# Kernel optimization log

Measured on AMD Instinct MI355X. Metric: run time of the kernel, lower is better.

The kernel has to match this reference:

```python
import jax, jax.numpy as jnp
import numpy as np
import math

B, T_TOK, D, H, L, V, NC, BS = 8, 511, 768, 12, 8, 512, 10, 512

PARAM_NAMES = ['tok_emb','cond_emb','type_emb','pos_emb','ln1_g','ln1_b','Wq','bq','Wk','bk','Wv','bv','Wp','bp','ln2_g','ln2_b','W1','b1','W2','b2','lnf_g','lnf_b','head_w']


def setup_inputs() -> dict:
    key = jax.random.key(0)
    ks = iter(jax.random.split(key, 40))
    def w(shape):
        return jax.random.normal(next(ks), shape, jnp.float32) * 0.02
    inp = {
        'idx': jax.random.randint(next(ks), (B, T_TOK), 0, V),
        'condition': jax.random.randint(next(ks), (B,), 0, NC + 1),
        'tok_emb': w((V, D)),
        'cond_emb': w((NC + 1, D)),
        'type_emb': w((2, D)),
        'pos_emb': w((1, BS, D)),
        'ln1_g': jnp.ones((L, D)), 'ln1_b': jnp.zeros((L, D)),
        'Wq': w((L, D, D)), 'bq': jnp.zeros((L, D)),
        'Wk': w((L, D, D)), 'bk': jnp.zeros((L, D)),
        'Wv': w((L, D, D)), 'bv': jnp.zeros((L, D)),
        'Wp': w((L, D, D)), 'bp': jnp.zeros((L, D)),
        'ln2_g': jnp.ones((L, D)), 'ln2_b': jnp.zeros((L, D)),
        'W1': w((L, D, 4 * D)), 'b1': jnp.zeros((L, 4 * D)),
        'W2': w((L, 4 * D, D)), 'b2': jnp.zeros((L, D)),
        'lnf_g': jnp.ones((D,)), 'lnf_b': jnp.zeros((D,)),
        'head_w': w((D, V)),
    }
    return inp


def _ln(x, g, b):
    m = x.mean(-1, keepdims=True)
    v = ((x - m) ** 2).mean(-1, keepdims=True)
    return (x - m) * jax.lax.rsqrt(v + 1e-5) * g + b


def _forward(idx, condition, p):
    b, t = idx.shape
    T = t + 1  # conditioning token prepended
    x = jnp.concatenate([p['cond_emb'][condition][:, None, :], p['tok_emb'][idx]], axis=1)
    type_ids = jnp.concatenate([jnp.zeros((1,), jnp.int32), jnp.ones((t,), jnp.int32)])
    x = x + p['pos_emb'][:, :T] + p['type_emb'][type_ids][None]
    dh = D // H
    causal = jnp.tril(jnp.ones((T, T), bool))

    def block(x, lp):
        ln1_g, ln1_b, Wq, bq, Wk, bk, Wv, bv, Wp, bp, ln2_g, ln2_b, W1, b1, W2, b2 = lp
        h = _ln(x, ln1_g, ln1_b)
        def heads(W, bias):
            return (h @ W + bias).reshape(b, T, H, dh).transpose(0, 2, 1, 3)  # [b,H,T,dh]
        q, k, v = heads(Wq, bq), heads(Wk, bk), heads(Wv, bv)
        att = jnp.einsum('bhqd,bhkd->bhqk', q, k) * (1.0 / math.sqrt(dh))
        att = jax.nn.softmax(jnp.where(causal, att, -jnp.inf), axis=-1)
        y = jnp.einsum('bhqk,bhkd->bhqd', att, v).transpose(0, 2, 1, 3).reshape(b, T, D)
        # NOTE: original Block applies ln1 in-place, so residual base is post-ln h
        x = h + (y @ Wp + bp)
        h2 = _ln(x, ln2_g, ln2_b)
        x = x + (jax.nn.gelu(h2 @ W1 + b1, approximate=False) @ W2 + b2)
        return x, None

    lp = (p['ln1_g'], p['ln1_b'], p['Wq'], p['bq'], p['Wk'], p['bk'], p['Wv'], p['bv'],
          p['Wp'], p['bp'], p['ln2_g'], p['ln2_b'], p['W1'], p['b1'], p['W2'], p['b2'])
    x, _ = jax.lax.scan(block, x, lp)
    logits = _ln(x, p['lnf_g'], p['lnf_b']) @ p['head_w']
    return logits[:, 1:, :]  # strip conditioning position (cond_len=1)


def reference(idx, condition, tok_emb, cond_emb, type_emb, pos_emb, ln1_g, ln1_b, Wq, bq, Wk, bk, Wv, bv, Wp, bp, ln2_g, ln2_b, W1, b1, W2, b2, lnf_g, lnf_b, head_w):
    p = dict(zip(PARAM_NAMES, (tok_emb, cond_emb, type_emb, pos_emb, ln1_g, ln1_b, Wq, bq, Wk, bk, Wv, bv, Wp, bp, ln2_g, ln2_b, W1, b1, W2, b2, lnf_g, lnf_b, head_w)))
    return _forward(idx, condition, p)
```

## Files before the change

### kernel.cpp

```cpp
#include <hip/hip_runtime.h>
#include <hip/hip_bf16.h>
#include <cstddef>
#include <cstdint>


#define NTOK 4096
#define TSEQ 512
#define DMODEL 768
#define DFF 3072
#define NHEAD 12
#define DHEAD 64
#define NLAYER 8
#define VOCAB 512
#define QKVD 2304

typedef __attribute__((ext_vector_type(8))) __bf16 bf16x8;
typedef __attribute__((ext_vector_type(4))) float f32x4;
typedef __attribute__((ext_vector_type(4))) unsigned int u32x4;
typedef __attribute__((ext_vector_type(4))) unsigned short u16x4;

__device__ __forceinline__ unsigned short f2bf(float f) {
  union { float f; unsigned int u; } v; v.f = f;
  return (unsigned short)((v.u + 0x7FFFu + ((v.u >> 16) & 1u)) >> 16);
}

__device__ __forceinline__ float gelu_exact(float x) {
  return 0.5f * x * (1.f + erff(x * 0.70710678118654752f));
}

__device__ __forceinline__ void gload_lds16(const void* g, void* lds) {
  __builtin_amdgcn_global_load_lds(
      reinterpret_cast<__attribute__((address_space(1))) void*>(
          reinterpret_cast<uintptr_t>(g)),
      reinterpret_cast<__attribute__((address_space(3))) void*>(
          reinterpret_cast<uintptr_t>(lds)),
      16, 0, 0);
}

__global__ __launch_bounds__(256) void embed_k(
    const int* __restrict__ idx, const int* __restrict__ cond,
    const float* __restrict__ tok, const float* __restrict__ ce,
    const float* __restrict__ te, const float* __restrict__ pe,
    float* __restrict__ X) {
  int row = blockIdx.x;
  int b = row >> 9, t = row & 511;
  int tid = threadIdx.x;
  const float* src = (t == 0) ? (ce + (size_t)cond[b] * DMODEL)
                              : (tok + (size_t)idx[b * 511 + t - 1] * DMODEL);
  const float* ty = te + (t != 0 ? DMODEL : 0);
  const float* pp = pe + (size_t)t * DMODEL;
  float* dst = X + (size_t)row * DMODEL;
#pragma unroll
  for (int i = 0; i < 3; i++) {
    int d = tid + i * 256;
    dst[d] = src[d] + pp[d] + ty[d];
  }
}

template <bool F32OUT>
__global__ __launch_bounds__(256) void ln_k(
    const float* __restrict__ X, const float* __restrict__ g,
    const float* __restrict__ bta, float* __restrict__ O,
    unsigned short* __restrict__ Ob) {
  const int row = blockIdx.x;
  const int tid = threadIdx.x;
  const float* x = X + (size_t)row * DMODEL;
  float v0 = x[tid], v1 = x[tid + 256], v2 = x[tid + 512];
  float s = v0 + v1 + v2;
  float ss = v0 * v0 + v1 * v1 + v2 * v2;
#pragma unroll
  for (int o = 32; o > 0; o >>= 1) {
    s += __shfl_down(s, o);
    ss += __shfl_down(ss, o);
  }
  __shared__ float sm[8];
  const int wid = tid >> 6, lane = tid & 63;
  if (lane == 0) { sm[wid] = s; sm[wid + 4] = ss; }
  __syncthreads();
  float st = sm[0] + sm[1] + sm[2] + sm[3];
  float sst = sm[4] + sm[5] + sm[6] + sm[7];
  float mean = st * (1.f / DMODEL);
  float var = sst * (1.f / DMODEL) - mean * mean;
  float rstd = rsqrtf(var + 1e-5f);
  float y0 = (v0 - mean) * rstd * g[tid] + bta[tid];
  float y1 = (v1 - mean) * rstd * g[tid + 256] + bta[tid + 256];
  float y2 = (v2 - mean) * rstd * g[tid + 512] + bta[tid + 512];
  if (F32OUT) {
    float* o = O + (size_t)row * DMODEL;
    o[tid] = y0; o[tid + 256] = y1; o[tid + 512] = y2;
  }
  unsigned short* ob = Ob + (size_t)row * DMODEL;
  ob[tid] = f2bf(y0); ob[tid + 256] = f2bf(y1); ob[tid + 512] = f2bf(y2);
}

struct P4 { const float* p[4]; };

__global__ __launch_bounds__(256) void transp_k(P4 src,
                                                unsigned short* __restrict__ out,
                                                int K, int N) {
  __shared__ alignas(16) float Ls[64][65];
  const float* W = src.p[blockIdx.z];
  unsigned short* o = out + (size_t)blockIdx.z * K * N;
  const int tid = threadIdx.x;
  const int n0 = blockIdx.x * 64, k0 = blockIdx.y * 64;
  const int r = tid >> 4, c4 = (tid & 15) * 4;
#pragma unroll
  for (int i = 0; i < 4; i++) {
    const int kk = r + i * 16;
    const float4 v = *(const float4*)(W + (size_t)(k0 + kk) * N + n0 + c4);
    Ls[c4 + 0][kk] = v.x;
    Ls[c4 + 1][kk] = v.y;
    Ls[c4 + 2][kk] = v.z;
    Ls[c4 + 3][kk] = v.w;
  }
  __syncthreads();
#pragma unroll
  for (int i = 0; i < 4; i++) {
    const int nn = r + i * 16;
    u16x4 q;
    q.x = f2bf(Ls[nn][c4 + 0]);
    q.y = f2bf(Ls[nn][c4 + 1]);
    q.z = f2bf(Ls[nn][c4 + 2]);
    q.w = f2bf(Ls[nn][c4 + 3]);
    *(u16x4*)(o + (size_t)(n0 + nn) * K + k0 + c4) = q;
  }
}

__global__ __launch_bounds__(256) void packb_k(const float* __restrict__ bq,
                                               const float* __restrict__ bk,
                                               const float* __restrict__ bv,
                                               float* __restrict__ o) {
  const int l = blockIdx.x, tid = threadIdx.x;
#pragma unroll
  for (int i = 0; i < 9; i++) {
    int n = tid + i * 256;
    float v = (n < 768) ? bq[l * 768 + n]
                        : (n < 1536) ? bk[l * 768 + n - 768]
                                     : bv[l * 768 + n - 1536];
    o[l * QKVD + n] = v;
  }
}

#define BK 32

constexpr int EPQ = 0;
constexpr int EPRES = 1;
constexpr int EPGELU = 2;
constexpr int EPHEAD = 3;
constexpr int EPQB = 4;

template <int EP, int TBM, int TBN>
__global__ __launch_bounds__(256) void mm_k(
    const unsigned short* __restrict__ A, const unsigned short* __restrict__ Bt,
    const float* __restrict__ bias, const float* __restrict__ res,
    void* __restrict__ Cv, int K, int N) {
  __shared__ alignas(16) unsigned short As[TBM * BK];
  __shared__ alignas(16) unsigned short Bs[TBN * BK];
  constexpr int WM = TBM / 2, WN = TBN / 2;
  constexpr int MI = WM / 16, NJ = WN / 16;
  const int tid = threadIdx.x;
  const int lane = tid & 63, wid = tid >> 6;
  const int wr = wid >> 1, wc = wid & 1;
  const int m0 = blockIdx.x * TBM, n0 = blockIdx.y * TBN;

  f32x4 acc[MI][NJ];
#pragma unroll
  for (int i = 0; i < MI; i++)
#pragma unroll
    for (int j = 0; j < NJ; j++) acc[i][j] = f32x4{0.f, 0.f, 0.f, 0.f};

  const int srow = lane >> 2;
  const int gch = (lane & 3) ^ ((srow >> 1) & 3);
  const size_t rb = (size_t)K * 2;
  const int fr = lane & 15, ks = lane >> 4;

  for (int k0 = 0; k0 < K; k0 += BK) {
#pragma unroll
    for (int t = 0; t < TBM / 64; t++) {
      const int rr = wid * (TBM / 4) + t * 16;
      gload_lds16((const char*)A + (size_t)(m0 + rr + srow) * rb +
                      (size_t)k0 * 2 + gch * 16,
                  As + rr * BK);
    }
#pragma unroll
    for (int t = 0; t < TBN / 64; t++) {
      const int rr = wid * (TBN / 4) + t * 16;
      gload_lds16((const char*)Bt + (size_t)(n0 + rr + srow) * rb +
                      (size_t)k0 * 2 + gch * 16,
                  Bs + rr * BK);
    }
    __syncthreads();

    u32x4 ar[MI], br[NJ];
#pragma unroll
    for (int i = 0; i < MI; i++) {
      const int ra = wr * WM + i * 16 + fr;
      ar[i] = *(const u32x4*)((const char*)As + ra * 64 +
                              ((ks ^ ((ra >> 1) & 3)) << 4));
    }
#pragma unroll
    for (int j = 0; j < NJ; j++) {
      const int rbw = wc * WN + j * 16 + fr;
      br[j] = *(const u32x4*)((const char*)Bs + rbw * 64 +
                              ((ks ^ ((rbw >> 1) & 3)) << 4));
    }
#pragma unroll
    for (int i = 0; i < MI; i++)
#pragma unroll
      for (int j = 0; j < NJ; j++)
        acc[i][j] = __builtin_amdgcn_mfma_f32_16x16x32_bf16(
            __builtin_bit_cast(bf16x8, ar[i]), __builtin_bit_cast(bf16x8, br[j]),
            acc[i][j], 0, 0, 0);
    __syncthreads();
  }

#pragma unroll
  for (int i = 0; i < MI; i++) {
#pragma unroll
    for (int j = 0; j < NJ; j++) {
      const int n = n0 + wc * WN + j * 16 + fr;
      float bv = 0.f;
      if (EP != EPHEAD) bv = bias[n];
#pragma unroll
      for (int r = 0; r < 4; r++) {
        const int m = m0 + wr * WM + i * 16 + ks * 4 + r;
        float v = acc[i][j][r] + bv;
        if (EP == EPRES) v += res[(size_t)m * N + n];
        if (EP == EPGELU) {
          ((unsigned short*)Cv)[(size_t)m * N + n] = f2bf(gelu_exact(v));
        } else if (EP == EPQB) {
          ((unsigned short*)Cv)[(size_t)m * N + n] = f2bf(v);
        } else if (EP == EPHEAD) {
          const int bb = m >> 9, tt = m & 511;
          if (tt)
            ((float*)Cv)[(size_t)(bb * 511 + tt - 1) * N + n] = v;
        } else {
          ((float*)Cv)[(size_t)m * N + n] = v;
        }
      }
    }
  }
}

__global__ __launch_bounds__(256) void attn_mfma_k(
    const unsigned short* __restrict__ QKV, unsigned short* __restrict__ Y) {
  __shared__ alignas(16) unsigned short Ks[64][72];
  __shared__ alignas(16) unsigned short Vt[64][72];
  __shared__ alignas(16) unsigned short Pl[4][16][72];
  const int qt = 7 - (int)blockIdx.x;
  const int h = blockIdx.y, b = blockIdx.z;
  const int tid = threadIdx.x;
  const int lane = tid & 63, wq = tid >> 6;
  const int fr = lane & 15, g = lane >> 4;

  const size_t qrow =
      (size_t)(b * TSEQ + qt * 64 + wq * 16 + fr) * QKVD + h * DHEAD;
  u32x4 qf[2];
  qf[0] = *(const u32x4*)(QKV + qrow + g * 8);
  qf[1] = *(const u32x4*)(QKV + qrow + 32 + g * 8);

  f32x4 of[4];
  float m[4], l[4];
#pragma unroll
  for (int jd = 0; jd < 4; jd++) of[jd] = f32x4{0.f, 0.f, 0.f, 0.f};
#pragma unroll
  for (int r = 0; r < 4; r++) { m[r] = -1e30f; l[r] = 0.f; }

  const int srow = tid >> 2, sc = (tid & 3) * 16;

  for (int kt = 0; kt <= qt; kt++) {
    {
      const size_t kr = (size_t)(b * TSEQ + kt * 64 + srow) * QKVD + h * DHEAD;
      u32x4 k0 = *(const u32x4*)(QKV + kr + DMODEL + sc);
      u32x4 k1 = *(const u32x4*)(QKV + kr + DMODEL + sc + 8);
      *(u32x4*)&Ks[srow][sc] = k0;
      *(u32x4*)&Ks[srow][sc + 8] = k1;
      u32x4 v0 = *(const u32x4*)(QKV + kr + 2 * DMODEL + sc);
      u32x4 v1 = *(const u32x4*)(QKV + kr + 2 * DMODEL + sc + 8);
      const unsigned short* vp = (const unsigned short*)&v0;
#pragma unroll
      for (int i = 0; i < 8; i++) Vt[sc + i][srow] = vp[i];
      vp = (const unsigned short*)&v1;
#pragma unroll
      for (int i = 0; i < 8; i++) Vt[sc + 8 + i][srow] = vp[i];
    }
    __syncthreads();

    f32x4 sf[4];
#pragma unroll
    for (int j = 0; j < 4; j++) sf[j] = f32x4{0.f, 0.f, 0.f, 0.f};
#pragma unroll
    for (int st = 0; st < 2; st++) {
#pragma unroll
      for (int j = 0; j < 4; j++) {
        u32x4 kf = *(const u32x4*)&Ks[j * 16 + fr][st * 32 + g * 8];
        sf[j] = __builtin_amdgcn_mfma_f32_16x16x32_bf16(
            __builtin_bit_cast(bf16x8, qf[st]), __builtin_bit_cast(bf16x8, kf),
            sf[j], 0, 0, 0);
      }
    }

    const bool diag = (kt == qt);
#pragma unroll
    for (int r = 0; r < 4; r++) {
      float pv[4];
      float mx = -1e30f;
#pragma unroll
      for (int j = 0; j < 4; j++) {
        float sv = sf[j][r] * 0.125f;
        if (diag && (j * 16 + fr > wq * 16 + g * 4 + r)) sv = -1e30f;
        pv[j] = sv;
        mx = fmaxf(mx, sv);
      }
      mx = fmaxf(mx, __shfl_xor(mx, 1));
      mx = fmaxf(mx, __shfl_xor(mx, 2));
      mx = fmaxf(mx, __shfl_xor(mx, 4));
      mx = fmaxf(mx, __shfl_xor(mx, 8));
      const float mn = fmaxf(m[r], mx);
      const float corr = __expf(m[r] - mn);
      m[r] = mn;
      float ls = 0.f;
#pragma unroll
      for (int j = 0; j < 4; j++) {
        const float e = __expf(pv[j] - mn);
        Pl[wq][g * 4 + r][j * 16 + fr] = f2bf(e);
        ls += e;
      }
      ls += __shfl_xor(ls, 1);
      ls += __shfl_xor(ls, 2);
      ls += __shfl_xor(ls, 4);
      ls += __shfl_xor(ls, 8);
      l[r] = l[r] * corr + ls;
#pragma unroll
      for (int jd = 0; jd < 4; jd++) of[jd][r] *= corr;
    }

#pragma unroll
    for (int st = 0; st < 2; st++) {
      u32x4 pf = *(const u32x4*)&Pl[wq][fr][st * 32 + g * 8];
#pragma unroll
      for (int jd = 0; jd < 4; jd++) {
        u32x4 vf = *(const u32x4*)&Vt[jd * 16 + fr][st * 32 + g * 8];
        of[jd] = __builtin_amdgcn_mfma_f32_16x16x32_bf16(
            __builtin_bit_cast(bf16x8, pf), __builtin_bit_cast(bf16x8, vf),
            of[jd], 0, 0, 0);
      }
    }
    __syncthreads();
  }

#pragma unroll
  for (int r = 0; r < 4; r++) {
    const float inv = 1.f / l[r];
    const size_t orow =
        (size_t)(b * TSEQ + qt * 64 + wq * 16 + g * 4 + r) * DMODEL + h * DHEAD;
#pragma unroll
    for (int jd = 0; jd < 4; jd++)
      Y[orow + jd * 16 + fr] = f2bf(of[jd][r] * inv);
  }
}

extern "C" void kernel_launch(void* const* d_in, const int* in_sizes, int n_in,
                              void* d_out, int out_size, void* d_ws, size_t ws_size,
                              hipStream_t stream) {
  const int* idx = (const int*)d_in[0];
  const int* condition = (const int*)d_in[1];
  const float* tok_emb = (const float*)d_in[2];
  const float* cond_emb = (const float*)d_in[3];
  const float* type_emb = (const float*)d_in[4];
  const float* pos_emb = (const float*)d_in[5];
  const float* ln1_g = (const float*)d_in[6];
  const float* ln1_b = (const float*)d_in[7];
  const float* Wq = (const float*)d_in[8];
  const float* bq = (const float*)d_in[9];
  const float* Wk = (const float*)d_in[10];
  const float* bk = (const float*)d_in[11];
  const float* Wv = (const float*)d_in[12];
  const float* bv = (const float*)d_in[13];
  const float* Wp = (const float*)d_in[14];
  const float* bp = (const float*)d_in[15];
  const float* ln2_g = (const float*)d_in[16];
  const float* ln2_b = (const float*)d_in[17];
  const float* W1 = (const float*)d_in[18];
  const float* b1 = (const float*)d_in[19];
  const float* W2 = (const float*)d_in[20];
  const float* b2 = (const float*)d_in[21];
  const float* lnf_g = (const float*)d_in[22];
  const float* lnf_b = (const float*)d_in[23];
  const float* head_w = (const float*)d_in[24];

  const size_t WDD = (size_t)DMODEL * DMODEL;
  const size_t WDF = (size_t)DMODEL * DFF;
  const size_t SD = (size_t)NTOK * DMODEL;

  char* wp = (char*)d_ws;
  auto alloc = [&](size_t bytes) {
    char* r = wp;
    wp += (bytes + 255) & ~(size_t)255;
    return r;
  };
  float* x = (float*)alloc(SD * 4);
  float* h = (float*)alloc(SD * 4);
  unsigned short* hb = (unsigned short*)alloc(SD * 2);
  unsigned short* big = (unsigned short*)alloc((size_t)NTOK * DFF * 2);
  unsigned short* qkv16 = big;
  unsigned short* m1b = big;
  unsigned short* yb = (unsigned short*)alloc(SD * 2);
  unsigned short* lw = (unsigned short*)alloc((4 * WDD + 2 * WDF) * 2);
  unsigned short* headt = (unsigned short*)alloc((size_t)VOCAB * DMODEL * 2);
  float* qkvb = (float*)alloc((size_t)NLAYER * QKVD * 4);

  unsigned short* lwQKV = lw;
  unsigned short* lwP = lw + 3 * WDD;
  unsigned short* lw1 = lw + 4 * WDD;
  unsigned short* lw2 = lw + 4 * WDD + WDF;

  embed_k<<<NTOK, 256, 0, stream>>>(idx, condition, tok_emb, cond_emb,
                                    type_emb, pos_emb, x);
  packb_k<<<NLAYER, 256, 0, stream>>>(bq, bk, bv, qkvb);
  {
    P4 s{{head_w, nullptr, nullptr, nullptr}};
    transp_k<<<dim3(VOCAB / 64, DMODEL / 64, 1), 256, 0, stream>>>(
        s, headt, DMODEL, VOCAB);
  }

  const dim3 gQKV(NTOK / 128, QKVD / 128);
  const dim3 gDD(NTOK / 128, DMODEL / 64);
  const dim3 gDF(NTOK / 128, DFF / 128);
  const dim3 gDV(NTOK / 128, VOCAB / 64);

  for (int l = 0; l < NLAYER; l++) {
    {
      P4 s{{Wq + l * WDD, Wk + l * WDD, Wv + l * WDD, Wp + l * WDD}};
      transp_k<<<dim3(12, 12, 4), 256, 0, stream>>>(s, lw, DMODEL, DMODEL);
      P4 s1{{W1 + l * WDF, nullptr, nullptr, nullptr}};
      transp_k<<<dim3(48, 12, 1), 256, 0, stream>>>(s1, lw1, DMODEL, DFF);
      P4 s2{{W2 + l * WDF, nullptr, nullptr, nullptr}};
      transp_k<<<dim3(12, 48, 1), 256, 0, stream>>>(s2, lw2, DFF, DMODEL);
    }
    ln_k<true><<<NTOK, 256, 0, stream>>>(x, ln1_g + l * DMODEL,
                                         ln1_b + l * DMODEL, h, hb);
    mm_k<EPQB, 128, 128><<<gQKV, 256, 0, stream>>>(
        hb, lwQKV, qkvb + l * QKVD, nullptr, qkv16, DMODEL, QKVD);
    attn_mfma_k<<<dim3(8, NHEAD, 8), 256, 0, stream>>>(qkv16, yb);
    mm_k<EPRES, 128, 64><<<gDD, 256, 0, stream>>>(
        yb, lwP, bp + l * DMODEL, h, x, DMODEL, DMODEL);
    ln_k<false><<<NTOK, 256, 0, stream>>>(x, ln2_g + l * DMODEL,
                                          ln2_b + l * DMODEL, nullptr, hb);
    mm_k<EPGELU, 128, 128><<<gDF, 256, 0, stream>>>(
        hb, lw1, b1 + l * DFF, nullptr, m1b, DMODEL, DFF);
    mm_k<EPRES, 128, 64><<<gDD, 256, 0, stream>>>(
        m1b, lw2, b2 + l * DMODEL, x, x, DFF, DMODEL);
  }

  ln_k<false><<<NTOK, 256, 0, stream>>>(x, lnf_g, lnf_b, nullptr, hb);
  mm_k<EPHEAD, 128, 64><<<gDV, 256, 0, stream>>>(
      hb, headt, nullptr, nullptr, d_out, DMODEL, VOCAB);
}
```

Before: 1.735 ms.

## Split-K with atomic residual accumulation, batch weight transposes across layers

Narrow-output GEMMs (projection, FFN2, head) now split K across blockIdx.z and accumulate into the residual stream with float atomics. The LayerNorm kernels pre-seed the residual buffer with the bias (and with the post-LN value for the attention residual), which removes the separate h buffer and the residual-read epilogue. All per-layer weight transposes are hoisted into three batched launches when the workspace is large enough. The aim is to raise occupancy on grids that had only 384 or 256 blocks and to cut launch count, at the cost of atomic traffic, nondeterministic summation order and an extra zeroing kernel for the output.

```diff
diff --git a/kernel.cpp b/kernel.cpp
--- a/kernel.cpp
+++ b/kernel.cpp
@@ -57,11 +57,11 @@
   }
 }
 
-template <bool F32OUT>
+template <int MODE>
 __global__ __launch_bounds__(256) void ln_k(
     const float* __restrict__ X, const float* __restrict__ g,
-    const float* __restrict__ bta, float* __restrict__ O,
-    unsigned short* __restrict__ Ob) {
+    const float* __restrict__ bta, unsigned short* __restrict__ Ob,
+    const float* __restrict__ eb, float* __restrict__ Xu) {
   const int row = blockIdx.x;
   const int tid = threadIdx.x;
   const float* x = X + (size_t)row * DMODEL;
@@ -85,9 +85,16 @@
   float y0 = (v0 - mean) * rstd * g[tid] + bta[tid];
   float y1 = (v1 - mean) * rstd * g[tid + 256] + bta[tid + 256];
   float y2 = (v2 - mean) * rstd * g[tid + 512] + bta[tid + 512];
-  if (F32OUT) {
-    float* o = O + (size_t)row * DMODEL;
-    o[tid] = y0; o[tid + 256] = y1; o[tid + 512] = y2;
+  if (MODE == 1) {
+    float* xu = Xu + (size_t)row * DMODEL;
+    xu[tid] = y0 + eb[tid];
+    xu[tid + 256] = y1 + eb[tid + 256];
+    xu[tid + 512] = y2 + eb[tid + 512];
+  } else if (MODE == 2) {
+    float* xu = Xu + (size_t)row * DMODEL;
+    xu[tid] = v0 + eb[tid];
+    xu[tid + 256] = v1 + eb[tid + 256];
+    xu[tid + 512] = v2 + eb[tid + 512];
   }
   unsigned short* ob = Ob + (size_t)row * DMODEL;
   ob[tid] = f2bf(y0); ob[tid + 256] = f2bf(y1); ob[tid + 512] = f2bf(y2);
@@ -97,10 +104,13 @@
 
 __global__ __launch_bounds__(256) void transp_k(P4 src,
                                                 unsigned short* __restrict__ out,
-                                                int K, int N) {
+                                                int K, int N, long srcL,
+                                                long dstL, int matsPer) {
   __shared__ alignas(16) float Ls[64][65];
-  const float* W = src.p[blockIdx.z];
-  unsigned short* o = out + (size_t)blockIdx.z * K * N;
+  const int z = blockIdx.z;
+  const int l = z / matsPer, mt = z - l * matsPer;
+  const float* W = src.p[mt] + (size_t)l * srcL;
+  unsigned short* o = out + (size_t)l * dstL + (size_t)mt * K * N;
   const int tid = threadIdx.x;
   const int n0 = blockIdx.x * 64, k0 = blockIdx.y * 64;
   const int r = tid >> 4, c4 = (tid & 15) * 4;
@@ -141,27 +151,35 @@
   }
 }
 
+__global__ __launch_bounds__(256) void zero_k(float* __restrict__ p) {
+  const size_t i = ((size_t)blockIdx.x * 256 + threadIdx.x) * 4;
+  *(f32x4*)(p + i) = f32x4{0.f, 0.f, 0.f, 0.f};
+}
+
 #define BK 32
 
 constexpr int EPQ = 0;
 constexpr int EPRES = 1;
 constexpr int EPGELU = 2;
-constexpr int EPHEAD = 3;
 constexpr int EPQB = 4;
+constexpr int EPATOM = 5;
+constexpr int EPATOMH = 6;
 
 template <int EP, int TBM, int TBN>
 __global__ __launch_bounds__(256) void mm_k(
     const unsigned short* __restrict__ A, const unsigned short* __restrict__ Bt,
     const float* __restrict__ bias, const float* __restrict__ res,
-    void* __restrict__ Cv, int K, int N) {
+    void* __restrict__ Cv, int K, int N, int kChunk) {
   __shared__ alignas(16) unsigned short As[TBM * BK];
   __shared__ alignas(16) unsigned short Bs[TBN * BK];
   constexpr int WM = TBM / 2, WN = TBN / 2;
   constexpr int MI = WM / 16, NJ = WN / 16;
+  constexpr bool HASB = (EP == EPQ || EP == EPRES || EP == EPGELU || EP == EPQB);
   const int tid = threadIdx.x;
   const int lane = tid & 63, wid = tid >> 6;
   const int wr = wid >> 1, wc = wid & 1;
   const int m0 = blockIdx.x * TBM, n0 = blockIdx.y * TBN;
+  const int kBeg = blockIdx.z * kChunk, kEnd = kBeg + kChunk;
 
   f32x4 acc[MI][NJ];
 #pragma unroll
@@ -174,7 +192,7 @@
   const size_t rb = (size_t)K * 2;
   const int fr = lane & 15, ks = lane >> 4;
 
-  for (int k0 = 0; k0 < K; k0 += BK) {
+  for (int k0 = kBeg; k0 < kEnd; k0 += BK) {
 #pragma unroll
     for (int t = 0; t < TBM / 64; t++) {
       const int rr = wid * (TBM / 4) + t * 16;
@@ -220,7 +238,7 @@
     for (int j = 0; j < NJ; j++) {
       const int n = n0 + wc * WN + j * 16 + fr;
       float bv = 0.f;
-      if (EP != EPHEAD) bv = bias[n];
+      if (HASB) bv = bias[n];
 #pragma unroll
       for (int r = 0; r < 4; r++) {
         const int m = m0 + wr * WM + i * 16 + ks * 4 + r;
@@ -230,10 +248,12 @@
           ((unsigned short*)Cv)[(size_t)m * N + n] = f2bf(gelu_exact(v));
         } else if (EP == EPQB) {
           ((unsigned short*)Cv)[(size_t)m * N + n] = f2bf(v);
-        } else if (EP == EPHEAD) {
+        } else if (EP == EPATOM) {
+          atomicAdd(&((float*)Cv)[(size_t)m * N + n], v);
+        } else if (EP == EPATOMH) {
           const int bb = m >> 9, tt = m & 511;
           if (tt)
-            ((float*)Cv)[(size_t)(bb * 511 + tt - 1) * N + n] = v;
+            atomicAdd(&((float*)Cv)[(size_t)(bb * 511 + tt - 1) * N + n], v);
         } else {
           ((float*)Cv)[(size_t)m * N + n] = v;
         }
@@ -392,6 +412,7 @@
   const size_t WDD = (size_t)DMODEL * DMODEL;
   const size_t WDF = (size_t)DMODEL * DFF;
   const size_t SD = (size_t)NTOK * DMODEL;
+  const size_t LW = 4 * WDD + 2 * WDF;
 
   char* wp = (char*)d_ws;
   auto alloc = [&](size_t bytes) {
@@ -400,20 +421,17 @@
     return r;
   };
   float* x = (float*)alloc(SD * 4);
-  float* h = (float*)alloc(SD * 4);
   unsigned short* hb = (unsigned short*)alloc(SD * 2);
   unsigned short* big = (unsigned short*)alloc((size_t)NTOK * DFF * 2);
   unsigned short* qkv16 = big;
   unsigned short* m1b = big;
   unsigned short* yb = (unsigned short*)alloc(SD * 2);
-  unsigned short* lw = (unsigned short*)alloc((4 * WDD + 2 * WDF) * 2);
   unsigned short* headt = (unsigned short*)alloc((size_t)VOCAB * DMODEL * 2);
   float* qkvb = (float*)alloc((size_t)NLAYER * QKVD * 4);
-
-  unsigned short* lwQKV = lw;
-  unsigned short* lwP = lw + 3 * WDD;
-  unsigned short* lw1 = lw + 4 * WDD;
-  unsigned short* lw2 = lw + 4 * WDD + WDF;
+  const size_t fixedB = (size_t)(wp - (char*)d_ws);
+  const bool bigws = ws_size >= fixedB + NLAYER * LW * 2 + 65536;
+  unsigned short* lw =
+      (unsigned short*)alloc((bigws ? NLAYER * LW : LW) * 2);
 
   embed_k<<<NTOK, 256, 0, stream>>>(idx, condition, tok_emb, cond_emb,
                                     type_emb, pos_emb, x);
@@ -421,39 +439,62 @@
   {
     P4 s{{head_w, nullptr, nullptr, nullptr}};
     transp_k<<<dim3(VOCAB / 64, DMODEL / 64, 1), 256, 0, stream>>>(
-        s, headt, DMODEL, VOCAB);
-  }
-
-  const dim3 gQKV(NTOK / 128, QKVD / 128);
-  const dim3 gDD(NTOK / 128, DMODEL / 64);
-  const dim3 gDF(NTOK / 128, DFF / 128);
-  const dim3 gDV(NTOK / 128, VOCAB / 64);
+        s, headt, DMODEL, VOCAB, 0, 0, 1);
+  }
+  if (bigws) {
+    P4 s{{Wq, Wk, Wv, Wp}};
+    transp_k<<<dim3(12, 12, 4 * NLAYER), 256, 0, stream>>>(
+        s, lw, DMODEL, DMODEL, (long)WDD, (long)LW, 4);
+    P4 s1{{W1, nullptr, nullptr, nullptr}};
+    transp_k<<<dim3(48, 12, NLAYER), 256, 0, stream>>>(
+        s1, lw + 4 * WDD, DMODEL, DFF, (long)WDF, (long)LW, 1);
+    P4 s2{{W2, nullptr, nullptr, nullptr}};
+    transp_k<<<dim3(12, 48, NLAYER), 256, 0, stream>>>(
+        s2, lw + 4 * WDD + WDF, DFF, DMODEL, (long)WDF, (long)LW, 1);
+  }
+
+  const dim3 gQKV(NTOK / 128, QKVD / 128, 1);
+  const dim3 gDD(NTOK / 128, DMODEL / 64, 2);
+  const dim3 gDF(NTOK / 128, DFF / 128, 1);
+  const dim3 gFF2(NTOK / 128, DMODEL / 64, 4);
+  const dim3 gDV(NTOK / 128, VOCAB / 64, 2);
 
   for (int l = 0; l < NLAYER; l++) {
-    {
+    unsigned short* lwL = lw + (bigws ? l * LW : 0);
+    unsigned short* lwQKV = lwL;
+    unsigned short* lwP = lwL + 3 * WDD;
+    unsigned short* lw1 = lwL + 4 * WDD;
+    unsigned short* lw2 = lwL + 4 * WDD + WDF;
+    if (!bigws) {
       P4 s{{Wq + l * WDD, Wk + l * WDD, Wv + l * WDD, Wp + l * WDD}};
-      transp_k<<<dim3(12, 12, 4), 256, 0, stream>>>(s, lw, DMODEL, DMODEL);
+      transp_k<<<dim3(12, 12, 4), 256, 0, stream>>>(s, lwL, DMODEL, DMODEL, 0,
+                                                    0, 4);
       P4 s1{{W1 + l * WDF, nullptr, nullptr, nullptr}};
-      transp_k<<<dim3(48, 12, 1), 256, 0, stream>>>(s1, lw1, DMODEL, DFF);
+      transp_k<<<dim3(48, 12, 1), 256, 0, stream>>>(s1, lw1, DMODEL, DFF, 0, 0,
+                                                    1);
       P4 s2{{W2 + l * WDF, nullptr, nullptr, nullptr}};
-      transp_k<<<dim3(12, 48, 1), 256, 0, stream>>>(s2, lw2, DFF, DMODEL);
-    }
-    ln_k<true><<<NTOK, 256, 0, stream>>>(x, ln1_g + l * DMODEL,
-                                         ln1_b + l * DMODEL, h, hb);
+      transp_k<<<dim3(12, 48, 1), 256, 0, stream>>>(s2, lw2, DFF, DMODEL, 0, 0,
+                                                    1);
+    }
+    ln_k<1><<<NTOK, 256, 0, stream>>>(x, ln1_g + l * DMODEL,
+                                      ln1_b + l * DMODEL, hb, bp + l * DMODEL,
+                                      x);
     mm_k<EPQB, 128, 128><<<gQKV, 256, 0, stream>>>(
-        hb, lwQKV, qkvb + l * QKVD, nullptr, qkv16, DMODEL, QKVD);
+        hb, lwQKV, qkvb + l * QKVD, nullptr, qkv16, DMODEL, QKVD, DMODEL);
     attn_mfma_k<<<dim3(8, NHEAD, 8), 256, 0, stream>>>(qkv16, yb);
-    mm_k<EPRES, 128, 64><<<gDD, 256, 0, stream>>>(
-        yb, lwP, bp + l * DMODEL, h, x, DMODEL, DMODEL);
-    ln_k<false><<<NTOK, 256, 0, stream>>>(x, ln2_g + l * DMODEL,
-                                          ln2_b + l * DMODEL, nullptr, hb);
+    mm_k<EPATOM, 128, 64><<<gDD, 256, 0, stream>>>(
+        yb, lwP, nullptr, nullptr, x, DMODEL, DMODEL, DMODEL / 2);
+    ln_k<2><<<NTOK, 256, 0, stream>>>(x, ln2_g + l * DMODEL,
+                                      ln2_b + l * DMODEL, hb, b2 + l * DMODEL,
+                                      x);
     mm_k<EPGELU, 128, 128><<<gDF, 256, 0, stream>>>(
-        hb, lw1, b1 + l * DFF, nullptr, m1b, DMODEL, DFF);
-    mm_k<EPRES, 128, 64><<<gDD, 256, 0, stream>>>(
-        m1b, lw2, b2 + l * DMODEL, x, x, DFF, DMODEL);
-  }
-
-  ln_k<false><<<NTOK, 256, 0, stream>>>(x, lnf_g, lnf_b, nullptr, hb);
-  mm_k<EPHEAD, 128, 64><<<gDV, 256, 0, stream>>>(
-      hb, headt, nullptr, nullptr, d_out, DMODEL, VOCAB);
-}
+        hb, lw1, b1 + l * DFF, nullptr, m1b, DMODEL, DFF, DMODEL);
+    mm_k<EPATOM, 128, 64><<<gFF2, 256, 0, stream>>>(
+        m1b, lw2, nullptr, nullptr, x, DFF, DMODEL, DFF / 4);
+  }
+
+  ln_k<0><<<NTOK, 256, 0, stream>>>(x, lnf_g, lnf_b, hb, nullptr, nullptr);
+  zero_k<<<out_size / 1024, 256, 0, stream>>>((float*)d_out);
+  mm_k<EPATOMH, 128, 64><<<gDV, 256, 0, stream>>>(
+      hb, headt, nullptr, nullptr, d_out, DMODEL, VOCAB, DMODEL / 2);
+}
```

Result: slower. 1.928 ms (+11.1%).
